# Kernel tuning notes

Measured on AMD Instinct MI355X. Metric: run time of the kernel, lower is better.

Reference implementation:

```python
import jax, jax.numpy as jnp
import numpy as np

D_MODEL = 1024
NUM_HEADS = 16
D_K = D_MODEL // NUM_HEADS
MAX_SEQ_LEN = 2048
THETA = 10000.0


def rotation_matrix_table(theta, d_k, max_seq_len):
    # [max_seq_len, d_k, d_k] block-diagonal 2x2 rotation matrices,
    # same math as the torch reference's generate_rotation_matrix.
    pos = jnp.arange(max_seq_len, dtype=jnp.float32)            # [S]
    kidx = jnp.arange(d_k // 2, dtype=jnp.float32)              # [d_k/2]
    angles = pos[:, None] / (theta ** (2.0 * kidx / d_k))       # [S, d_k/2]
    cos, sin = jnp.cos(angles), jnp.sin(angles)
    rot = jnp.zeros((max_seq_len, d_k, d_k), dtype=jnp.float32)
    ev = jnp.arange(0, d_k, 2)
    od = ev + 1
    rot = rot.at[:, ev, ev].set(cos)
    rot = rot.at[:, ev, od].set(-sin)
    rot = rot.at[:, od, ev].set(sin)
    rot = rot.at[:, od, od].set(cos)
    return rot


def setup_inputs() -> dict:
    key = jax.random.key(0)
    k0, k1, k2, k3, k4 = jax.random.split(key, 5)
    B, S = 4, 2048
    std = np.sqrt(2.0 / (D_MODEL + D_MODEL))
    return {
        "in_features": jax.random.normal(k0, (B, S, D_MODEL), dtype=jnp.float32),
        "wq": jax.random.normal(k1, (D_MODEL, D_MODEL), dtype=jnp.float32) * std,
        "wk": jax.random.normal(k2, (D_MODEL, D_MODEL), dtype=jnp.float32) * std,
        "wv": jax.random.normal(k3, (D_MODEL, D_MODEL), dtype=jnp.float32) * std,
        "wo": jax.random.normal(k4, (D_MODEL, D_MODEL), dtype=jnp.float32) * std,
    }


def reference(in_features, wq, wk, wv, wo):
    B, S, _ = in_features.shape
    H, Dk = NUM_HEADS, D_K
    # QKV projections (weights stored [out, in], applied as x @ W.T)
    q = in_features @ wq.T
    k = in_features @ wk.T
    v = in_features @ wv.T
    # [B, H, S, Dk]
    q = q.reshape(B, S, H, Dk).transpose(0, 2, 1, 3)
    k = k.reshape(B, S, H, Dk).transpose(0, 2, 1, 3)
    v = v.reshape(B, S, H, Dk).transpose(0, 2, 1, 3)
    # RoPE via dense per-position rotation matrix (faithful to source)
    rot = rotation_matrix_table(THETA, Dk, MAX_SEQ_LEN)[:S]     # [S, Dk, Dk]
    q = jnp.einsum("sde,bhse->bhsd", rot, q)
    k = jnp.einsum("sde,bhse->bhsd", rot, k)
    # scaled dot-product attention with causal mask
    scores = jnp.einsum("bhqd,bhkd->bhqk", q, k) / np.sqrt(Dk)
    causal = jnp.tril(jnp.ones((S, S), dtype=bool))             # True = keep
    scores = jnp.where(causal[None, None], scores, -jnp.inf)
    attn = jax.nn.softmax(scores, axis=-1)
    out = jnp.einsum("bhqk,bhkd->bhqd", attn, v)
    out = out.transpose(0, 2, 1, 3).reshape(B, S, H * Dk)
    return out @ wo.T
```

## Files before the change

kernel.cpp:

```cpp
#include <hip/hip_runtime.h>

#define SEQ     2048
#define DMODEL  1024
#define NHEADS  16
#define DKH     64
#define BATCH   4

typedef __bf16 bf16x8 __attribute__((ext_vector_type(8)));
typedef float  f32x4  __attribute__((ext_vector_type(4)));

static __device__ __forceinline__ unsigned short f2bf(float x) {
  unsigned int u = __float_as_uint(x);
  u += 0x7fffu + ((u >> 16) & 1u);
  return (unsigned short)(u >> 16);
}
static __device__ __forceinline__ float bf2f(unsigned short b) {
  return __uint_as_float(((unsigned int)b) << 16);
}
static __device__ __forceinline__ void gload_lds16(const void* g, void* lds) {
  __builtin_amdgcn_global_load_lds((const __attribute__((address_space(1))) void*)g,
                                   (__attribute__((address_space(3))) void*)lds,
                                   16, 0, 0);
}
static __device__ __forceinline__ f32x4 mfma16(bf16x8 a, bf16x8 b, f32x4 c) {
  return __builtin_amdgcn_mfma_f32_16x16x32_bf16(a, b, c, 0, 0, 0);
}

__global__ void cast_kernel(const float* __restrict__ src,
                            unsigned short* __restrict__ dst, int n4) {
  int i = blockIdx.x * 256 + threadIdx.x;
  if (i >= n4) return;
  float4 v = ((const float4*)src)[i];
  ushort4 o;
  o.x = f2bf(v.x); o.y = f2bf(v.y); o.z = f2bf(v.z); o.w = f2bf(v.w);
  ((ushort4*)dst)[i] = o;
}

__global__ void cast4_kernel(const float* __restrict__ s0, const float* __restrict__ s1,
                             const float* __restrict__ s2, const float* __restrict__ s3,
                             unsigned short* __restrict__ d0, unsigned short* __restrict__ d1,
                             unsigned short* __restrict__ d2, unsigned short* __restrict__ d3,
                             int n4) {
  int i = blockIdx.x * 256 + threadIdx.x;
  if (i >= n4) return;
  const float* s = (blockIdx.y == 0) ? s0 : (blockIdx.y == 1) ? s1 : (blockIdx.y == 2) ? s2 : s3;
  unsigned short* d = (blockIdx.y == 0) ? d0 : (blockIdx.y == 1) ? d1 : (blockIdx.y == 2) ? d2 : d3;
  float4 v = ((const float4*)s)[i];
  ushort4 o;
  o.x = f2bf(v.x); o.y = f2bf(v.y); o.z = f2bf(v.z); o.w = f2bf(v.w);
  ((ushort4*)d)[i] = o;
}

template<int EPI>
__global__ __launch_bounds__(256)
void gemm_bt(const unsigned short* __restrict__ A,
             const unsigned short* __restrict__ W0,
             const unsigned short* __restrict__ W1,
             const unsigned short* __restrict__ W2,
             unsigned short* __restrict__ O0,
             unsigned short* __restrict__ O1,
             unsigned short* __restrict__ O2,
             float* __restrict__ Of)
{
  __shared__ unsigned short sA[2][128*64];
  __shared__ unsigned short sB[2][128*64];
  const int tid = threadIdx.x;
  const int lane = tid & 63, w = tid >> 6;
  const int wm = w >> 1, wn = w & 1;
  const int li = lane & 15, lg = lane >> 4;

  const int NWG = (EPI == 0) ? 1536 : 512;
  const int CPX = NWG / 8;
  const int lgid = (blockIdx.x & 7) * CPX + (blockIdx.x >> 3);
  const int n0 = (lgid & 7) * 128;
  const int m0 = ((lgid >> 3) & 63) * 128;
  const int z  = (EPI == 0) ? (lgid >> 9) : 0;
  const unsigned short* Bw = (EPI == 0)
      ? ((z == 0) ? W0 : ((z == 1) ? W1 : W2)) : W0;

  const f32x4 fz = {0.f, 0.f, 0.f, 0.f};
  f32x4 acc[4][4];
  #pragma unroll
  for (int a = 0; a < 4; ++a)
    #pragma unroll
    for (int b = 0; b < 4; ++b)
      acc[a][b] = fz;

  auto STAGE = [&](int buf, int t) {
    const int k0 = t * 64;
    #pragma unroll
    for (int it = 0; it < 4; ++it) {
      int c = it*4 + w;
      int off16 = c*64 + lane;
      int r = off16 >> 3, p = off16 & 7;
      int s = p ^ (r & 7);
      gload_lds16(A  + (size_t)(m0 + r)*DMODEL + k0 + s*8, (char*)sA[buf] + c*1024);
      gload_lds16(Bw + (size_t)(n0 + r)*DMODEL + k0 + s*8, (char*)sB[buf] + c*1024);
    }
  };

  const int NT = DMODEL / 64;
  STAGE(0, 0);
  STAGE(1, 1);

  for (int t = 0; t < NT; ++t) {
    const int cur = t & 1;
    if (t == NT - 1) asm volatile("s_waitcnt vmcnt(0)" ::: "memory");
    else             asm volatile("s_waitcnt vmcnt(8)" ::: "memory");
    __builtin_amdgcn_s_barrier();
    __builtin_amdgcn_sched_barrier(0);

    #pragma unroll
    for (int kf = 0; kf < 2; ++kf) {
      bf16x8 af[4], bfr[4];
      #pragma unroll
      for (int mi = 0; mi < 4; ++mi) {
        int rr = wm*64 + mi*16 + li;
        int sp = (kf*4 + lg) ^ (rr & 7);
        af[mi] = *(const bf16x8*)(sA[cur] + rr*64 + sp*8);
      }
      #pragma unroll
      for (int ni = 0; ni < 4; ++ni) {
        int rr = wn*64 + ni*16 + li;
        int sp = (kf*4 + lg) ^ (rr & 7);
        bfr[ni] = *(const bf16x8*)(sB[cur] + rr*64 + sp*8);
      }
      __builtin_amdgcn_s_setprio(1);
      #pragma unroll
      for (int mi = 0; mi < 4; ++mi)
        #pragma unroll
        for (int ni = 0; ni < 4; ++ni)
          acc[mi][ni] = mfma16(af[mi], bfr[ni], acc[mi][ni]);
      __builtin_amdgcn_s_setprio(0);
    }

    __builtin_amdgcn_sched_barrier(0);
    __builtin_amdgcn_s_barrier();
    __builtin_amdgcn_sched_barrier(0);
    if (t + 2 < NT) STAGE(cur, t + 2);
  }

  unsigned short* Odst = O0;
  if (EPI == 0) Odst = (z == 0) ? O0 : ((z == 1) ? O1 : O2);

  float invf[4];
  if (EPI == 0) {
    #pragma unroll
    for (int ni = 0; ni < 4; ++ni) {
      int i_of = (ni*16 + li) >> 1;
      invf[ni] = exp2f(-0.41524101186092029f * (float)i_of);
    }
  }

  #pragma unroll
  for (int mi = 0; mi < 4; ++mi) {
    #pragma unroll
    for (int ni = 0; ni < 4; ++ni) {
      #pragma unroll
      for (int r = 0; r < 4; ++r) {
        int m = m0 + wm*64 + mi*16 + lg*4 + r;
        int n = n0 + wn*64 + ni*16 + li;
        float v = acc[mi][ni][r];
        if (EPI == 0) {
          int b = m >> 11, sq = m & (SEQ-1), hh = n >> 6, dk = n & 63;
          float prt = __shfl_xor(v, 1);
          if (z == 2) {
            Odst[(((size_t)b*NHEADS + hh)*DKH + dk)*SEQ + sq] = f2bf(v);
          } else {
            float ang = (float)sq * invf[ni];
            float sn, cs;
            __sincosf(ang, &sn, &cs);
            float out = (li & 1) ? (sn*prt + cs*v) : (cs*v - sn*prt);
            if (z == 0) out *= 0.18033688011112043f;
            Odst[(((size_t)b*NHEADS + hh)*SEQ + sq)*DKH + dk] = f2bf(out);
          }
        } else {
          Of[(size_t)m*DMODEL + n] = v;
        }
      }
    }
  }
}

__global__ __launch_bounds__(512)
void attn_kernel(const unsigned short* __restrict__ Qg,
                 const unsigned short* __restrict__ Kg,
                 const unsigned short* __restrict__ Vtg,
                 unsigned short* __restrict__ Og)
{
  const int lgid = (blockIdx.x & 7) * 64 + (blockIdx.x >> 3);
  const int px = lgid & 7;
  const int bh = lgid >> 3;
  const int tid = threadIdx.x;
  const int lane = tid & 63, w = tid >> 6;
  const int li = lane & 15, lg = lane >> 4;
  const float THRL2 = 11.0f;

  __shared__ unsigned short sK[2][64*64];
  __shared__ unsigned short sV[2][64*64];
  __shared__ unsigned short sP[8][16*72];
  unsigned short* sPw = sP[w];

  const size_t bhBase = (size_t)bh * SEQ * DKH;

  bf16x8 onesf;
  {
    __bf16 ob = (__bf16)1.0f;
    #pragma unroll
    for (int j = 0; j < 8; ++j) onesf[j] = ob;
  }
  const f32x4 fz = {0.f, 0.f, 0.f, 0.f};

  auto STAGE = [&](int buf, int t) {
    const int kv0 = t * 64;
    int off16 = w*64 + lane;
    int r = off16 >> 3, p = off16 & 7;
    int s = p ^ (r & 7);
    gload_lds16(Kg  + bhBase + (size_t)(kv0 + r)*DKH + s*8, (char*)sK[buf] + w*1024);
    gload_lds16(Vtg + bhBase + (size_t)r*SEQ + kv0 + s*8,   (char*)sV[buf] + w*1024);
  };

  #pragma unroll 1
  for (int pass = 0; pass < 2; ++pass) {
    const int qt = pass ? (15 - px) : px;
    const int q0 = qt * 128;
    const int myrow0 = q0 + w*16;

    bf16x8 qf[2];
    {
      const unsigned short* qp = Qg + bhBase + (size_t)(myrow0 + li)*DKH + lg*8;
      qf[0] = *(const bf16x8*)qp;
      qf[1] = *(const bf16x8*)(qp + 32);
    }

    f32x4 acc_o[4], ls4;
    float m_r[4];
    #pragma unroll
    for (int nt = 0; nt < 4; ++nt) acc_o[nt] = fz;
    ls4 = fz;
    #pragma unroll
    for (int kr = 0; kr < 4; ++kr) m_r[kr] = -1e30f;

    const int nt_stage = 2*qt + 2;
    const int last_t  = 2*qt + (w >= 4 ? 1 : 0);

    STAGE(0, 0);
    STAGE(1, 1);

    for (int t = 0; t < nt_stage; ++t) {
      const int cur = t & 1;
      if (t == nt_stage - 1) asm volatile("s_waitcnt vmcnt(0)" ::: "memory");
      else                   asm volatile("s_waitcnt vmcnt(2)" ::: "memory");
      __builtin_amdgcn_s_barrier();
      __builtin_amdgcn_sched_barrier(0);

      if (t <= last_t) {
        const int kv0 = t * 64;
        f32x4 sc[4];
        #pragma unroll
        for (int nt = 0; nt < 4; ++nt) sc[nt] = fz;
        __builtin_amdgcn_s_setprio(1);
        #pragma unroll
        for (int kf = 0; kf < 2; ++kf) {
          #pragma unroll
          for (int nt = 0; nt < 4; ++nt) {
            int row = nt*16 + li;
            int sp = (kf*4 + lg) ^ (row & 7);
            bf16x8 kb = *(const bf16x8*)(sK[cur] + row*64 + sp*8);
            sc[nt] = mfma16(qf[kf], kb, sc[nt]);
          }
        }
        __builtin_amdgcn_s_setprio(0);

        if (t == last_t) {
          #pragma unroll
          for (int nt = 0; nt < 4; ++nt)
            #pragma unroll
            for (int kr = 0; kr < 4; ++kr) {
              int col = kv0 + nt*16 + li;
              int row = myrow0 + lg*4 + kr;
              if (col > row) sc[nt][kr] = -1e30f;
            }
        }

        float pm[4];
        #pragma unroll
        for (int kr = 0; kr < 4; ++kr)
          pm[kr] = fmaxf(fmaxf(sc[0][kr], sc[1][kr]), fmaxf(sc[2][kr], sc[3][kr]));
        int need = (pm[0] > m_r[0] + THRL2) | (pm[1] > m_r[1] + THRL2) |
                   (pm[2] > m_r[2] + THRL2) | (pm[3] > m_r[3] + THRL2);
        if (__any(need)) {
          #pragma unroll
          for (int kr = 0; kr < 4; ++kr) {
            float m2 = pm[kr];
            m2 = fmaxf(m2, __shfl_xor(m2, 1));
            m2 = fmaxf(m2, __shfl_xor(m2, 2));
            m2 = fmaxf(m2, __shfl_xor(m2, 4));
            m2 = fmaxf(m2, __shfl_xor(m2, 8));
            float mn = fmaxf(m_r[kr], m2);
            float scl = __builtin_amdgcn_exp2f(m_r[kr] - mn);
            m_r[kr] = mn;
            #pragma unroll
            for (int nt = 0; nt < 4; ++nt) acc_o[nt][kr] *= scl;
            ls4[kr] *= scl;
          }
        }
        #pragma unroll
        for (int nt = 0; nt < 4; ++nt)
          #pragma unroll
          for (int kr = 0; kr < 4; ++kr)
            sc[nt][kr] = __builtin_amdgcn_exp2f(sc[nt][kr] - m_r[kr]);

        #pragma unroll
        for (int nt = 0; nt < 4; ++nt)
          #pragma unroll
          for (int kr = 0; kr < 4; ++kr)
            sPw[(lg*4 + kr)*72 + nt*16 + li] = f2bf(sc[nt][kr]);

        bf16x8 pa[2];
        #pragma unroll
        for (int kf = 0; kf < 2; ++kf)
          pa[kf] = *(const bf16x8*)(sPw + li*72 + kf*32 + lg*8);

        __builtin_amdgcn_s_setprio(1);
        ls4 = mfma16(pa[0], onesf, ls4);
        ls4 = mfma16(pa[1], onesf, ls4);
        #pragma unroll
        for (int kf = 0; kf < 2; ++kf)
          #pragma unroll
          for (int nt = 0; nt < 4; ++nt) {
            int rr = nt*16 + li;
            int sp = (kf*4 + lg) ^ (rr & 7);
            bf16x8 vb = *(const bf16x8*)(sV[cur] + rr*64 + sp*8);
            acc_o[nt] = mfma16(pa[kf], vb, acc_o[nt]);
          }
        __builtin_amdgcn_s_setprio(0);
      }

      __builtin_amdgcn_sched_barrier(0);
      __builtin_amdgcn_s_barrier();
      __builtin_amdgcn_sched_barrier(0);
      if (t + 2 < nt_stage) STAGE(cur, t + 2);
    }

    const int b = bh >> 4, hh = bh & 15;
    #pragma unroll
    for (int kr = 0; kr < 4; ++kr) {
      float inv = __builtin_amdgcn_rcpf(ls4[kr]);
      int srow = myrow0 + lg*4 + kr;
      size_t orow = ((size_t)b*SEQ + srow)*DMODEL + (size_t)hh*DKH;
      #pragma unroll
      for (int nt = 0; nt < 4; ++nt)
        Og[orow + nt*16 + li] = f2bf(acc_o[nt][kr] * inv);
    }
  }
}

extern "C" void kernel_launch(void* const* d_in, const int* in_sizes, int n_in,
                              void* d_out, int out_size, void* d_ws, size_t ws_size,
                              hipStream_t stream)
{
  (void)in_sizes; (void)n_in; (void)out_size; (void)ws_size;
  const float* X  = (const float*)d_in[0];
  const float* Wq = (const float*)d_in[1];
  const float* Wk = (const float*)d_in[2];
  const float* Wv = (const float*)d_in[3];
  const float* Wo = (const float*)d_in[4];

  char* ws = (char*)d_ws;
  const size_t SZ_X = (size_t)8192 * 1024 * 2;
  const size_t SZ_W = (size_t)1024 * 1024 * 2;
  unsigned short* Xb  = (unsigned short*)(ws);
  unsigned short* Wqb = (unsigned short*)(ws + SZ_X);
  unsigned short* Wkb = (unsigned short*)(ws + SZ_X + 1*SZ_W);
  unsigned short* Wvb = (unsigned short*)(ws + SZ_X + 2*SZ_W);
  unsigned short* Wob = (unsigned short*)(ws + SZ_X + 3*SZ_W);
  unsigned short* Vtb = (unsigned short*)(ws + SZ_X + 4*SZ_W);
  unsigned short* Qb  = (unsigned short*)d_out;
  unsigned short* Kb  = Qb + (size_t)8192 * 1024;
  unsigned short* Ob  = Xb;

  cast_kernel<<<8192, 256, 0, stream>>>(X, Xb, 8388608/4);
  cast4_kernel<<<dim3(1024, 4), 256, 0, stream>>>(Wq, Wk, Wv, Wo,
                                                  Wqb, Wkb, Wvb, Wob, 1048576/4);

  gemm_bt<0><<<1536, 256, 0, stream>>>(Xb, Wqb, Wkb, Wvb, Qb, Kb, Vtb, nullptr);
  attn_kernel<<<512, 512, 0, stream>>>(Qb, Kb, Vtb, Ob);
  gemm_bt<1><<<512, 256, 0, stream>>>(Ob, Wob, nullptr, nullptr,
                                      nullptr, nullptr, nullptr,
                                      (float*)d_out);
}
```

Measured before the change: 192.8 us.

## Switch GEMM to 32x32x16 MFMA and stage V-transpose epilogue through LDS

The projection GEMM inner loop now uses 32x32x16 bf16 MFMA tiles (2x2 per wave) instead of 16x16x32 (4x4 per wave). This halves the LDS fragment reads per k-step and the number of MFMA issues. The V output, which is written transposed, is now staged through shared memory and written as 16-byte contiguous rows instead of scattered 2-byte strided stores. The RoPE and fp32 epilogues are remapped to the 32x32 accumulator layout.

New measurement: 169.6 us. 1.14x faster.

```diff
diff --git a/kernel.cpp b/kernel.cpp
--- a/kernel.cpp
+++ b/kernel.cpp
@@ -8,6 +8,7 @@
 
 typedef __bf16 bf16x8 __attribute__((ext_vector_type(8)));
 typedef float  f32x4  __attribute__((ext_vector_type(4)));
+typedef float  f32x16 __attribute__((ext_vector_type(16)));
 
 static __device__ __forceinline__ unsigned short f2bf(float x) {
   unsigned int u = __float_as_uint(x);
@@ -24,6 +25,9 @@
 }
 static __device__ __forceinline__ f32x4 mfma16(bf16x8 a, bf16x8 b, f32x4 c) {
   return __builtin_amdgcn_mfma_f32_16x16x32_bf16(a, b, c, 0, 0, 0);
+}
+static __device__ __forceinline__ f32x16 mfma32(bf16x8 a, bf16x8 b, f32x16 c) {
+  return __builtin_amdgcn_mfma_f32_32x32x16_bf16(a, b, c, 0, 0, 0);
 }
 
 __global__ void cast_kernel(const float* __restrict__ src,
@@ -62,12 +66,11 @@
              unsigned short* __restrict__ O2,
              float* __restrict__ Of)
 {
-  __shared__ unsigned short sA[2][128*64];
-  __shared__ unsigned short sB[2][128*64];
+  __shared__ unsigned short smem[4][128*64];
   const int tid = threadIdx.x;
   const int lane = tid & 63, w = tid >> 6;
   const int wm = w >> 1, wn = w & 1;
-  const int li = lane & 15, lg = lane >> 4;
+  const int l31 = lane & 31, lg2 = lane >> 5;
 
   const int NWG = (EPI == 0) ? 1536 : 512;
   const int CPX = NWG / 8;
@@ -78,13 +81,14 @@
   const unsigned short* Bw = (EPI == 0)
       ? ((z == 0) ? W0 : ((z == 1) ? W1 : W2)) : W0;
 
-  const f32x4 fz = {0.f, 0.f, 0.f, 0.f};
-  f32x4 acc[4][4];
+  f32x16 acc[2][2];
   #pragma unroll
-  for (int a = 0; a < 4; ++a)
-    #pragma unroll
-    for (int b = 0; b < 4; ++b)
-      acc[a][b] = fz;
+  for (int a = 0; a < 2; ++a)
+    #pragma unroll
+    for (int b = 0; b < 2; ++b)
+      #pragma unroll
+      for (int r = 0; r < 16; ++r)
+        acc[a][b][r] = 0.f;
 
   auto STAGE = [&](int buf, int t) {
     const int k0 = t * 64;
@@ -94,8 +98,8 @@
       int off16 = c*64 + lane;
       int r = off16 >> 3, p = off16 & 7;
       int s = p ^ (r & 7);
-      gload_lds16(A  + (size_t)(m0 + r)*DMODEL + k0 + s*8, (char*)sA[buf] + c*1024);
-      gload_lds16(Bw + (size_t)(n0 + r)*DMODEL + k0 + s*8, (char*)sB[buf] + c*1024);
+      gload_lds16(A  + (size_t)(m0 + r)*DMODEL + k0 + s*8, (char*)smem[buf]     + c*1024);
+      gload_lds16(Bw + (size_t)(n0 + r)*DMODEL + k0 + s*8, (char*)smem[2 + buf] + c*1024);
     }
   };
 
@@ -111,26 +115,26 @@
     __builtin_amdgcn_sched_barrier(0);
 
     #pragma unroll
-    for (int kf = 0; kf < 2; ++kf) {
-      bf16x8 af[4], bfr[4];
-      #pragma unroll
-      for (int mi = 0; mi < 4; ++mi) {
-        int rr = wm*64 + mi*16 + li;
-        int sp = (kf*4 + lg) ^ (rr & 7);
-        af[mi] = *(const bf16x8*)(sA[cur] + rr*64 + sp*8);
+    for (int ks = 0; ks < 4; ++ks) {
+      bf16x8 af[2], bg[2];
+      #pragma unroll
+      for (int bi = 0; bi < 2; ++bi) {
+        int row = wm*64 + bi*32 + l31;
+        int sp = (ks*2 + lg2) ^ (row & 7);
+        af[bi] = *(const bf16x8*)((const char*)smem[cur] + row*128 + sp*16);
       }
       #pragma unroll
-      for (int ni = 0; ni < 4; ++ni) {
-        int rr = wn*64 + ni*16 + li;
-        int sp = (kf*4 + lg) ^ (rr & 7);
-        bfr[ni] = *(const bf16x8*)(sB[cur] + rr*64 + sp*8);
+      for (int bj = 0; bj < 2; ++bj) {
+        int row = wn*64 + bj*32 + l31;
+        int sp = (ks*2 + lg2) ^ (row & 7);
+        bg[bj] = *(const bf16x8*)((const char*)smem[2 + cur] + row*128 + sp*16);
       }
       __builtin_amdgcn_s_setprio(1);
       #pragma unroll
-      for (int mi = 0; mi < 4; ++mi)
-        #pragma unroll
-        for (int ni = 0; ni < 4; ++ni)
-          acc[mi][ni] = mfma16(af[mi], bfr[ni], acc[mi][ni]);
+      for (int bi = 0; bi < 2; ++bi)
+        #pragma unroll
+        for (int bj = 0; bj < 2; ++bj)
+          acc[bi][bj] = mfma32(af[bi], bg[bj], acc[bi][bj]);
       __builtin_amdgcn_s_setprio(0);
     }
 
@@ -140,45 +144,76 @@
     if (t + 2 < NT) STAGE(cur, t + 2);
   }
 
-  unsigned short* Odst = O0;
-  if (EPI == 0) Odst = (z == 0) ? O0 : ((z == 1) ? O1 : O2);
-
-  float invf[4];
-  if (EPI == 0) {
-    #pragma unroll
-    for (int ni = 0; ni < 4; ++ni) {
-      int i_of = (ni*16 + li) >> 1;
-      invf[ni] = exp2f(-0.41524101186092029f * (float)i_of);
-    }
+  if (EPI == 1) {
+    #pragma unroll
+    for (int bi = 0; bi < 2; ++bi)
+      #pragma unroll
+      for (int bj = 0; bj < 2; ++bj)
+        #pragma unroll
+        for (int r = 0; r < 16; ++r) {
+          int m = m0 + wm*64 + bi*32 + (r & 3) + 8*(r >> 2) + 4*lg2;
+          int n = n0 + wn*64 + bj*32 + l31;
+          Of[(size_t)m*DMODEL + n] = acc[bi][bj][r];
+        }
+    return;
   }
 
-  #pragma unroll
-  for (int mi = 0; mi < 4; ++mi) {
-    #pragma unroll
-    for (int ni = 0; ni < 4; ++ni) {
-      #pragma unroll
-      for (int r = 0; r < 4; ++r) {
-        int m = m0 + wm*64 + mi*16 + lg*4 + r;
-        int n = n0 + wn*64 + ni*16 + li;
-        float v = acc[mi][ni][r];
-        if (EPI == 0) {
+  unsigned short* Odst = (z == 0) ? O0 : ((z == 1) ? O1 : O2);
+
+  if (z == 2) {
+    unsigned short* tb = (unsigned short*)smem;
+    #pragma unroll
+    for (int bi = 0; bi < 2; ++bi)
+      #pragma unroll
+      for (int bj = 0; bj < 2; ++bj) {
+        int n_loc = wn*64 + bj*32 + l31;
+        #pragma unroll
+        for (int g = 0; g < 4; ++g) {
+          int m_loc = wm*64 + bi*32 + 8*g + 4*lg2;
+          ushort4 pk;
+          pk.x = f2bf(acc[bi][bj][g*4 + 0]);
+          pk.y = f2bf(acc[bi][bj][g*4 + 1]);
+          pk.z = f2bf(acc[bi][bj][g*4 + 2]);
+          pk.w = f2bf(acc[bi][bj][g*4 + 3]);
+          *(ushort4*)(tb + n_loc*136 + m_loc) = pk;
+        }
+      }
+    __syncthreads();
+    const int bb  = m0 >> 11;
+    const int sq0 = m0 & (SEQ - 1);
+    const size_t obase = (size_t)bb * NHEADS * DKH * SEQ;
+    #pragma unroll
+    for (int it = 0; it < 8; ++it) {
+      int nn = it*16 + (tid >> 4);
+      int cc = tid & 15;
+      bf16x8 v8 = *(const bf16x8*)(tb + nn*136 + cc*8);
+      int hh = (n0 + nn) >> 6;
+      int dk = nn & 63;
+      *(bf16x8*)&Odst[obase + ((size_t)hh*DKH + dk)*SEQ + sq0 + cc*8] = v8;
+    }
+  } else {
+    float invf2[2];
+    #pragma unroll
+    for (int bj = 0; bj < 2; ++bj)
+      invf2[bj] = exp2f(-0.41524101186092029f * (float)((bj*32 + l31) >> 1));
+    #pragma unroll
+    for (int bi = 0; bi < 2; ++bi)
+      #pragma unroll
+      for (int bj = 0; bj < 2; ++bj)
+        #pragma unroll
+        for (int r = 0; r < 16; ++r) {
+          int m = m0 + wm*64 + bi*32 + (r & 3) + 8*(r >> 2) + 4*lg2;
+          int n = n0 + wn*64 + bj*32 + l31;
+          float v = acc[bi][bj][r];
           int b = m >> 11, sq = m & (SEQ-1), hh = n >> 6, dk = n & 63;
           float prt = __shfl_xor(v, 1);
-          if (z == 2) {
-            Odst[(((size_t)b*NHEADS + hh)*DKH + dk)*SEQ + sq] = f2bf(v);
-          } else {
-            float ang = (float)sq * invf[ni];
-            float sn, cs;
-            __sincosf(ang, &sn, &cs);
-            float out = (li & 1) ? (sn*prt + cs*v) : (cs*v - sn*prt);
-            if (z == 0) out *= 0.18033688011112043f;
-            Odst[(((size_t)b*NHEADS + hh)*SEQ + sq)*DKH + dk] = f2bf(out);
-          }
-        } else {
-          Of[(size_t)m*DMODEL + n] = v;
-        }
-      }
-    }
+          float ang = (float)sq * invf2[bj];
+          float sn, cs;
+          __sincosf(ang, &sn, &cs);
+          float out = (l31 & 1) ? (sn*prt + cs*v) : (cs*v - sn*prt);
+          if (z == 0) out *= 0.18033688011112043f;
+          Odst[(((size_t)b*NHEADS + hh)*SEQ + sq)*DKH + dk] = f2bf(out);
+        }
   }
 }
 
```
